# Performance work log

Hardware: AMD Instinct MI355X
Metric: run time of the kernel (lower is better)

The kernel has to match this reference:

```python
import jax, jax.numpy as jnp
import numpy as np

B, D = 90000, 100
E_GNN, E_MLP = 4, 4
E = E_GNN + E_MLP + 1  # 9
K = 2
NOISE_EPS = 0.01
LOSS_COEF = 0.4
GATE_MEAN, GATE_STD = 0.1, 1.0  # registered buffers in the torch module


def setup_inputs() -> dict:
    key = jax.random.key(0)
    ks = jax.random.split(key, 16)
    f = jax.random.normal
    return {
        "memory_feats": f(ks[0], (B, D), jnp.float32),
        "recent_raw": f(ks[1], (B, E_MLP, D), jnp.float32),
        "spatial_raw": f(ks[2], (B, E_GNN, D), jnp.float32),
        "node_feats_src": f(ks[3], (B, D), jnp.float32),
        "noise": f(ks[4], (B, E), jnp.float32),
        "deg_coef": f(ks[5], (1, D, 2), jnp.float32),
        "w_gate": f(ks[6], (6 * D, E), jnp.float32) * 0.05,
        "w_noise": f(ks[7], (6 * D, E), jnp.float32) * 0.05,
        "src_w": f(ks[8], (D, D), jnp.float32) * 0.1,
        "src_b": f(ks[9], (D,), jnp.float32) * 0.1,
        "dst_w": f(ks[10], (D, D), jnp.float32) * 0.1,
        "dst_b": f(ks[11], (D,), jnp.float32) * 0.1,
        "out_w": f(ks[12], (D, 1), jnp.float32) * 0.1,
        "out_b": f(ks[13], (1,), jnp.float32) * 0.1,
        "degree": jax.random.randint(ks[14], (B,), 0, 64, jnp.int32),
        "neg_samples": 1,
    }


def _cv_squared(x):
    # torch .var() is unbiased (ddof=1)
    return jnp.var(x, ddof=1) / (jnp.mean(x) ** 2 + 1e-10)


def _norm_cdf(v):
    return jax.scipy.stats.norm.cdf(v, loc=GATE_MEAN, scale=GATE_STD)


def reference(memory_feats, recent_raw, spatial_raw, node_feats_src, noise,
              deg_coef, w_gate, w_noise, src_w, src_b, dst_w, dst_b,
              out_w, out_b, degree, neg_samples):
    # memory expert output (dropout is identity in eval; relu applied)
    mem = jax.nn.relu(memory_feats)                        # [B, D]
    rec = jax.nn.relu(recent_raw)                          # [B, Em, D]
    log_deg = jnp.log(degree.astype(mem.dtype) + 1.0)      # [B]
    # degree-conditioned reweighting: stack([r, r*log_deg],-1) * deg_coef, sum(-1)
    c0, c1 = deg_coef[0, :, 0], deg_coef[0, :, 1]          # [D]
    spa = spatial_raw * (c0 + log_deg[:, None, None] * c1)  # [B, Eg, D]

    combine = jnp.concatenate([mem[:, None, :], spa, rec], axis=1)  # [B, E, D]
    result_spa = spa.mean(axis=1)
    result_rec = rec.mean(axis=1)
    x1 = mem + result_spa + result_rec
    x2 = mem * result_spa * result_rec
    cat = jnp.concatenate([mem, result_spa, result_rec, x1, x2, node_feats_src], axis=1)  # [B, 6D]

    # noisy top-k gating (train=True)
    clean = cat @ w_gate                                   # [B, E]
    std = jax.nn.softplus(cat @ w_noise) + NOISE_EPS
    noisy = clean + noise * std
    top_vals, top_idx = jax.lax.top_k(noisy, K + 1)        # [B, K+1]
    topk_gates = jax.nn.softmax(top_vals[:, :K], axis=1)
    b_idx = jnp.arange(noisy.shape[0])[:, None]
    gates = jnp.zeros_like(noisy).at[b_idx, top_idx[:, :K]].set(topk_gates)

    # prob of being in top-k for load-balance loss
    thr_in = top_vals[:, K][:, None]
    thr_out = top_vals[:, K - 1][:, None]
    is_in = noisy > thr_in
    prob = jnp.where(is_in,
                     _norm_cdf((clean - thr_in) / std),
                     _norm_cdf((clean - thr_out) / std))
    load = prob.sum(axis=0)
    importance = gates.sum(axis=0)
    loss = LOSS_COEF * (_cv_squared(importance) + _cv_squared(load))

    out = jnp.einsum('bed,be->bd', combine, gates)         # [B, D]

    # edge predictor
    num_edge = out.shape[0] // (neg_samples + 2)
    h_src = out[:num_edge] @ src_w + src_b
    h_pos = out[num_edge:2 * num_edge] @ dst_w + dst_b
    h_neg = out[2 * num_edge:] @ dst_w + dst_b
    pos = jax.nn.relu(h_src + h_pos) @ out_w + out_b       # [num_edge, 1]
    neg = jax.nn.relu(jnp.tile(h_src, (neg_samples, 1)) + h_neg) @ out_w + out_b
    return pos, neg, loss
```

## Files before the change

### kernel.cpp

```cpp
#include <hip/hip_runtime.h>
#include <math.h>

#define DD 100
#define GGATE 1024

#define DPP_ADD(v, ctrl) ((v) + __int_as_float(__builtin_amdgcn_update_dpp( \
    0, __float_as_int(v), (ctrl), 0xf, 0xf, true)))

__device__ __forceinline__ float blo(unsigned u){
  union { unsigned i; float f; } c; c.i = u << 16; return c.f;
}
__device__ __forceinline__ float bhi(unsigned u){
  union { unsigned i; float f; } c; c.i = u & 0xFFFF0000u; return c.f;
}
__device__ __forceinline__ unsigned short f2bf(float f){
  unsigned u = __float_as_uint(f);
  unsigned r = (u + 0x7FFFu + ((u >> 16) & 1u)) >> 16;
  return (unsigned short)r;
}
__device__ __forceinline__ float phi_fast(float z){
  float x  = z * 0.70710678118654752440f;
  float ax = fabsf(x);
  float t  = __builtin_amdgcn_rcpf(1.0f + 0.3275911f*ax);
  float p  = t*(0.254829592f + t*(-0.284496736f + t*(1.421413741f
           + t*(-1.453152027f + t*1.061405429f))));
  float e  = __expf(-ax*ax);
  float erfv = copysignf(1.0f - p*e, x);
  return 0.5f*(1.0f + erfv);
}
__device__ __forceinline__ float4 relu4(float4 v){
  return make_float4(fmaxf(v.x,0.f), fmaxf(v.y,0.f), fmaxf(v.z,0.f), fmaxf(v.w,0.f));
}

__global__ void k_fold(const float* __restrict__ wg, const float* __restrict__ wn,
                       float* __restrict__ wfold)
{
  int idx = blockIdx.x*256 + threadIdx.x;
  if (idx >= 9000) return;
  int dim = idx/90, r = idx%90, s = r/18, e = r%18;
  const float* W = (e < 9) ? wg : wn;
  int ee = (e < 9) ? e : e-9;
  int rowA = (s==0) ? dim : (s==1) ? 100+dim : (s==2) ? 200+dim
           : (s==3) ? 400+dim : 500+dim;
  float v = W[rowA*9 + ee] + ((s < 3) ? W[(300+dim)*9 + ee] : 0.f);
  wfold[idx] = v;
}

__global__ __launch_bounds__(256) void k_gate(
    const float* __restrict__ memf, const float* __restrict__ recr,
    const float* __restrict__ spar, const float* __restrict__ nsrc,
    const float* __restrict__ noise, const float* __restrict__ degc,
    const float* __restrict__ wfold, const int* __restrict__ degree,
    float4* __restrict__ gateinfo, float* __restrict__ partials, int B)
{
  __shared__ __align__(16) float sWF[100*92];
  __shared__ __align__(16) float sC0[DD], sC1[DD];
  __shared__ float sPart[4][18];

  for (int i = threadIdx.x; i < 9000; i += 256){
    int d = i/90, r = i%90;
    int slot = (d>>2) + 25*(d&3);
    sWF[slot*92 + r] = wfold[i];
  }
  for (int i = threadIdx.x; i < DD; i += 256){ sC0[i]=degc[2*i]; sC1[i]=degc[2*i+1]; }
  __syncthreads();

  const int wave = threadIdx.x >> 6, lane = threadIdx.x & 63;
  const int fq = lane & 3, rl = lane >> 2;
  const float4* sC04 = (const float4*)sC0;
  const float4* sC14 = (const float4*)sC1;

  float ldA[9], imA[9];
  #pragma unroll
  for (int e = 0; e < 9; e++){ ldA[e]=0.f; imA[e]=0.f; }

  const int ntile = (B + 63) / 64;
  for (int t = blockIdx.x; t < ntile; t += GGATE){
    const int row = t*64 + wave*16 + rl;
    const bool valid = row < B;
    const int rc = valid ? row : B-1;
    const float* pm = memf + (size_t)rc*DD;
    const float* ps = spar + (size_t)rc*4*DD;
    const float* pr = recr + (size_t)rc*4*DD;
    const float* pn = nsrc + (size_t)rc*DD;
    float ldg = __logf((float)degree[rc] + 1.0f);

    float cg[9], cn[9];
    #pragma unroll
    for (int e = 0; e < 9; e++){ cg[e]=0.f; cn[e]=0.f; }

    for (int k = 0; k < 7; k++){
      int c = fq + 4*k;
      float fz = (c < 25) ? 1.f : 0.f;
      int ce = (c < 25) ? c : 0;
      float4 me = *(const float4*)(pm + 4*ce);
      float4 s0 = *(const float4*)(ps + 0*DD + 4*ce);
      float4 s1 = *(const float4*)(ps + 1*DD + 4*ce);
      float4 s2 = *(const float4*)(ps + 2*DD + 4*ce);
      float4 s3 = *(const float4*)(ps + 3*DD + 4*ce);
      float4 r0 = *(const float4*)(pr + 0*DD + 4*ce);
      float4 r1 = *(const float4*)(pr + 1*DD + 4*ce);
      float4 r2 = *(const float4*)(pr + 2*DD + 4*ce);
      float4 r3 = *(const float4*)(pr + 3*DD + 4*ce);
      float4 nv = *(const float4*)(pn + 4*ce);
      float4 c04 = sC04[ce], c14 = sC14[ce];

      float4 m4 = relu4(me);
      float4 sc = make_float4(c04.x + ldg*c14.x, c04.y + ldg*c14.y,
                              c04.z + ldg*c14.z, c04.w + ldg*c14.w);
      float4 rs4 = make_float4((s0.x+s1.x+s2.x+s3.x)*0.25f*sc.x,
                               (s0.y+s1.y+s2.y+s3.y)*0.25f*sc.y,
                               (s0.z+s1.z+s2.z+s3.z)*0.25f*sc.z,
                               (s0.w+s1.w+s2.w+s3.w)*0.25f*sc.w);
      float4 a0 = relu4(r0), a1 = relu4(r1), a2 = relu4(r2), a3 = relu4(r3);
      float4 rr4 = make_float4((a0.x+a1.x+a2.x+a3.x)*0.25f,
                               (a0.y+a1.y+a2.y+a3.y)*0.25f,
                               (a0.z+a1.z+a2.z+a3.z)*0.25f,
                               (a0.w+a1.w+a2.w+a3.w)*0.25f);
      m4.x*=fz; m4.y*=fz; m4.z*=fz; m4.w*=fz;
      rs4.x*=fz; rs4.y*=fz; rs4.z*=fz; rs4.w*=fz;
      rr4.x*=fz; rr4.y*=fz; rr4.z*=fz; rr4.w*=fz;
      float4 ns4 = make_float4(nv.x*fz, nv.y*fz, nv.z*fz, nv.w*fz);
      float4 x24 = make_float4(m4.x*rs4.x*rr4.x, m4.y*rs4.y*rr4.y,
                               m4.z*rs4.z*rr4.z, m4.w*rs4.w*rr4.w);

      #pragma unroll
      for (int j = 0; j < 4; j++){
        const float der0 = (j==0)?m4.x :(j==1)?m4.y :(j==2)?m4.z :m4.w;
        const float der1 = (j==0)?rs4.x:(j==1)?rs4.y:(j==2)?rs4.z:rs4.w;
        const float der2 = (j==0)?rr4.x:(j==1)?rr4.y:(j==2)?rr4.z:rr4.w;
        const float der3 = (j==0)?x24.x:(j==1)?x24.y:(j==2)?x24.z:x24.w;
        const float der4 = (j==0)?ns4.x:(j==1)?ns4.y:(j==2)?ns4.z:ns4.w;
        const float4* wpj = (const float4*)(sWF + (ce + 25*j)*92);
        #pragma unroll
        for (int tq = 0; tq < 23; tq++){
          float4 w = wpj[tq];
          #pragma unroll
          for (int u = 0; u < 4; u++){
            const int ww = 4*tq + u;
            if (ww < 90){
              const int seg = ww/18, e = ww%18;
              float wv = (u==0)?w.x:(u==1)?w.y:(u==2)?w.z:w.w;
              float dv = (seg==0)?der0:(seg==1)?der1:(seg==2)?der2:(seg==3)?der3:der4;
              if (e < 9) cg[e] += dv*wv; else cn[e-9] += dv*wv;
            }
          }
        }
      }
    }

    #pragma unroll
    for (int e = 0; e < 9; e++){
      cg[e] = DPP_ADD(cg[e], 0xB1); cg[e] = DPP_ADD(cg[e], 0x4E);
      cn[e] = DPP_ADD(cn[e], 0xB1); cn[e] = DPP_ADD(cn[e], 0x4E);
    }

    float sd[9], rsd[9], nz[9];
    #pragma unroll
    for (int e = 0; e < 9; e++){
      float x = cn[e];
      float spl = fmaxf(x, 0.f) + __logf(1.0f + __expf(-fabsf(x)));
      sd[e]  = spl + 0.01f;
      rsd[e] = __builtin_amdgcn_rcpf(sd[e]);
      nz[e]  = cg[e] + noise[(size_t)rc*9 + e] * sd[e];
    }
    float v1 = -3.402823e38f, v2 = v1, v3 = v1; int i1 = -1, i2 = -1;
    #pragma unroll
    for (int e = 0; e < 9; e++){
      float v = nz[e];
      if (v > v1){ v3=v2; v2=v1; i2=i1; v1=v; i1=e; }
      else if (v > v2){ v3=v2; v2=v; i2=e; }
      else if (v > v3){ v3=v; }
    }
    float tt = __expf(v2 - v1);
    float g1 = __builtin_amdgcn_rcpf(1.0f + tt);
    float g2 = tt*g1;
    if (valid){
      #pragma unroll
      for (int e = 0; e < 9; e++){
        float thr = (nz[e] > v3) ? v3 : v2;
        float z = (cg[e] - thr)*rsd[e] - 0.1f;
        ldA[e] += phi_fast(z);
        imA[e] += (e==i1) ? g1 : ((e==i2) ? g2 : 0.f);
      }
      if (fq == 0)
        gateinfo[row] = make_float4(g1, g2, __int_as_float(i1), __int_as_float(i2));
    }
  }

  #pragma unroll
  for (int e = 0; e < 9; e++){
    #pragma unroll
    for (int off = 4; off < 64; off <<= 1){
      ldA[e] += __shfl_xor(ldA[e], off, 64);
      imA[e] += __shfl_xor(imA[e], off, 64);
    }
  }
  if (lane == 0){
    #pragma unroll
    for (int e = 0; e < 9; e++){ sPart[wave][e] = imA[e]; sPart[wave][9+e] = ldA[e]; }
  }
  __syncthreads();
  if (threadIdx.x < 18){
    float s = sPart[0][threadIdx.x] + sPart[1][threadIdx.x]
            + sPart[2][threadIdx.x] + sPart[3][threadIdx.x];
    partials[blockIdx.x*18 + threadIdx.x] = s;
  }
}

__global__ __launch_bounds__(256) void k_mix(
    const float* __restrict__ memf, const float* __restrict__ recr,
    const float* __restrict__ spar, const float* __restrict__ degc,
    const int* __restrict__ degree, const float4* __restrict__ gateinfo,
    float* __restrict__ outm, int B)
{
  const int total = B*25;
  for (int idx = blockIdx.x*256 + threadIdx.x; idx < total; idx += gridDim.x*256){
    int row = idx / 25, q = idx - row*25;
    float4 gi = gateinfo[row];
    float gv[2] = {gi.x, gi.y};
    int   ei[2] = {__float_as_int(gi.z), __float_as_int(gi.w)};
    float4 acc = make_float4(0.f,0.f,0.f,0.f);
    #pragma unroll
    for (int s = 0; s < 2; s++){
      int e = ei[s]; float g = gv[s];
      float4 v;
      if (e == 0){
        v = relu4(*(const float4*)(memf + (size_t)row*DD + 4*q));
      } else if (e < 5){
        float ldg = __logf((float)degree[row] + 1.0f);
        float4 ca = *(const float4*)(degc + 8*q);
        float4 cb = *(const float4*)(degc + 8*q + 4);
        float4 sv = *(const float4*)(spar + ((size_t)row*4 + (e-1))*DD + 4*q);
        v = make_float4(sv.x*(ca.x + ldg*ca.y), sv.y*(ca.z + ldg*ca.w),
                        sv.z*(cb.x + ldg*cb.y), sv.w*(cb.z + ldg*cb.w));
      } else {
        v = relu4(*(const float4*)(recr + ((size_t)row*4 + (e-5))*DD + 4*q));
      }
      acc.x += g*v.x; acc.y += g*v.y; acc.z += g*v.z; acc.w += g*v.w;
    }
    ((float4*)outm)[(size_t)row*25 + q] = acc;
  }
}

__global__ __launch_bounds__(1024) void k_loss(const float* __restrict__ partials,
                                               int nblk, float* __restrict__ dloss)
{
  __shared__ float sS[18][57];
  int t = threadIdx.x;
  if (t < 1008){
    int k = t % 18, c = t / 18;
    float s = 0.f;
    for (int b = c; b < nblk; b += 56) s += partials[b*18 + k];
    sS[k][c] = s;
  }
  __syncthreads();
  if (t < 18){
    float tot = 0.f;
    #pragma unroll
    for (int c = 0; c < 56; c++) tot += sS[t][c];
    sS[t][56] = tot;
  }
  __syncthreads();
  if (t == 0){
    float mi = 0.f, ml = 0.f;
    #pragma unroll
    for (int e = 0; e < 9; e++){ mi += sS[e][56]; ml += sS[9+e][56]; }
    mi *= (1.f/9.f); ml *= (1.f/9.f);
    float vi = 0.f, vl = 0.f;
    #pragma unroll
    for (int e = 0; e < 9; e++){
      float a = sS[e][56]   - mi; vi += a*a;
      float b = sS[9+e][56] - ml; vl += b*b;
    }
    vi *= (1.f/8.f); vl *= (1.f/8.f);
    *dloss = 0.4f * (vi/(mi*mi + 1e-10f) + vl/(ml*ml + 1e-10f));
  }
}

__global__ __launch_bounds__(512) void k_edge(
    const float* __restrict__ om,
    const float* __restrict__ sw, const float* __restrict__ sb,
    const float* __restrict__ dw, const float* __restrict__ db,
    const float* __restrict__ ow, const float* __restrict__ ob,
    float* __restrict__ dout, int NE)
{
  __shared__ __align__(4) unsigned short sSW[DD*102];
  __shared__ __align__(4) unsigned short sDW[DD*102];
  __shared__ float sSB[DD], sDB[DD], sOW[DD];

  for (int i = threadIdx.x; i < DD*DD; i += 512){
    int k = i / DD, d = i % DD;
    sSW[d*102 + k] = f2bf(sw[i]);
    sDW[d*102 + k] = f2bf(dw[i]);
  }
  for (int i = threadIdx.x; i < DD; i += 512){ sSB[i]=sb[i]; sDB[i]=db[i]; sOW[i]=ow[i]; }
  __syncthreads();

  const int wave = threadIdx.x >> 6, lane = threadIdx.x & 63;
  const int grp = blockIdx.x*8 + wave;
  const int e0 = grp*4;
  if (e0 >= NE) return;
  const int e0u = __builtin_amdgcn_readfirstlane(e0);
  const float* oS = om + (size_t)e0u*DD;
  const float* oP = om + ((size_t)(NE  + e0u))*DD;
  const float* oN = om + ((size_t)(2*NE + e0u))*DD;
  const int d0 = lane, d1 = lane + 64;
  const bool h1 = (d1 < DD);
  const int dc1 = h1 ? d1 : 0;

  float aS[4][2], aP[4][2], aN[4][2];
  #pragma unroll
  for (int r = 0; r < 4; r++){
    aS[r][0]=0.f; aS[r][1]=0.f; aP[r][0]=0.f; aP[r][1]=0.f; aN[r][0]=0.f; aN[r][1]=0.f;
  }

  for (int k = 0; k < DD; k += 4){
    unsigned uA = *(const unsigned*)&sSW[d0 *102 + k];
    unsigned uB = *(const unsigned*)&sSW[d0 *102 + k + 2];
    unsigned uC = *(const unsigned*)&sSW[dc1*102 + k];
    unsigned uD = *(const unsigned*)&sSW[dc1*102 + k + 2];
    unsigned uE = *(const unsigned*)&sDW[d0 *102 + k];
    unsigned uF = *(const unsigned*)&sDW[d0 *102 + k + 2];
    unsigned uG = *(const unsigned*)&sDW[dc1*102 + k];
    unsigned uH = *(const unsigned*)&sDW[dc1*102 + k + 2];
    float wS00=blo(uA), wS01=bhi(uA), wS02=blo(uB), wS03=bhi(uB);
    float wS10=blo(uC), wS11=bhi(uC), wS12=blo(uD), wS13=bhi(uD);
    float wD00=blo(uE), wD01=bhi(uE), wD02=blo(uF), wD03=bhi(uF);
    float wD10=blo(uG), wD11=bhi(uG), wD12=blo(uH), wD13=bhi(uH);
    #pragma unroll
    for (int r = 0; r < 4; r++){
      float4 ov = *(const float4*)(oS + r*DD + k);
      float4 pv = *(const float4*)(oP + r*DD + k);
      float4 nv = *(const float4*)(oN + r*DD + k);
      aS[r][0] += ov.x*wS00 + ov.y*wS01 + ov.z*wS02 + ov.w*wS03;
      aS[r][1] += ov.x*wS10 + ov.y*wS11 + ov.z*wS12 + ov.w*wS13;
      aP[r][0] += pv.x*wD00 + pv.y*wD01 + pv.z*wD02 + pv.w*wD03;
      aP[r][1] += pv.x*wD10 + pv.y*wD11 + pv.z*wD12 + pv.w*wD13;
      aN[r][0] += nv.x*wD00 + nv.y*wD01 + nv.z*wD02 + nv.w*wD03;
      aN[r][1] += nv.x*wD10 + nv.y*wD11 + nv.z*wD12 + nv.w*wD13;
    }
  }

  float owa = sOW[d0], owb = sOW[dc1];
  float sba = sSB[d0], sbb = sSB[dc1];
  float dba = sDB[d0], dbb = sDB[dc1];
  float ob0 = ob[0];
  #pragma unroll
  for (int r = 0; r < 4; r++){
    float hs0 = aS[r][0] + sba, hp0 = aP[r][0] + dba, hn0 = aN[r][0] + dba;
    float tp = fmaxf(hs0 + hp0, 0.f)*owa;
    float tn = fmaxf(hs0 + hn0, 0.f)*owa;
    if (h1){
      float hs1 = aS[r][1] + sbb, hp1 = aP[r][1] + dbb, hn1 = aN[r][1] + dbb;
      tp += fmaxf(hs1 + hp1, 0.f)*owb;
      tn += fmaxf(hs1 + hn1, 0.f)*owb;
    }
    #pragma unroll
    for (int off = 32; off > 0; off >>= 1){
      tp += __shfl_xor(tp, off, 64);
      tn += __shfl_xor(tn, off, 64);
    }
    if (lane == 0){
      dout[e0 + r]      = tp + ob0;
      dout[NE + e0 + r] = tn + ob0;
    }
  }
}

extern "C" void kernel_launch(void* const* d_in, const int* in_sizes, int n_in,
                              void* d_out, int out_size, void* d_ws, size_t ws_size,
                              hipStream_t stream)
{
  (void)n_in; (void)out_size; (void)ws_size;
  const float* memf  = (const float*)d_in[0];
  const float* recr  = (const float*)d_in[1];
  const float* spar  = (const float*)d_in[2];
  const float* nsrc  = (const float*)d_in[3];
  const float* noise = (const float*)d_in[4];
  const float* degc  = (const float*)d_in[5];
  const float* wg    = (const float*)d_in[6];
  const float* wn    = (const float*)d_in[7];
  const float* sw    = (const float*)d_in[8];
  const float* sb    = (const float*)d_in[9];
  const float* dw    = (const float*)d_in[10];
  const float* db    = (const float*)d_in[11];
  const float* ow    = (const float*)d_in[12];
  const float* ob    = (const float*)d_in[13];
  const int*   deg   = (const int*)d_in[14];

  const int B  = in_sizes[0] / DD;
  const int NE = B / 3;

  float4* gateinfo = (float4*)d_ws;
  float*  outm     = (float*)(gateinfo + B);
  float*  partials = outm + (size_t)B*DD;
  float*  wfold    = partials + (size_t)GGATE*18;
  float*  dout     = (float*)d_out;

  k_fold<<<dim3(36), dim3(256), 0, stream>>>(wg, wn, wfold);
  k_gate<<<dim3(GGATE), dim3(256), 0, stream>>>(memf, recr, spar, nsrc, noise,
                                                degc, wfold, deg, gateinfo,
                                                partials, B);
  k_mix<<<dim3(2048), dim3(256), 0, stream>>>(memf, recr, spar, degc, deg,
                                              gateinfo, outm, B);
  k_loss<<<dim3(1), dim3(1024), 0, stream>>>(partials, GGATE, dout + 2*NE);
  const int blocks2 = (NE/4 + 7) / 8;
  k_edge<<<dim3(blocks2), dim3(512), 0, stream>>>(outm, sw, sb, dw, db, ow, ob, dout, NE);
}
```

Measured before the change: 257.1 us.

## Fuse expert mixing into gating kernel and software-prefetch next input chunk

Removes the separate k_mix kernel and the gateinfo buffer. Each row's gated mixture is now computed inside k_gate right after top-k selection, while the row's data is likely still in cache. The 7-step feature loop also double-buffers its global loads, issuing the next chunk's ten float4 loads before the FMA-heavy inner work, with the loop kept rolled. This saves one launch and a global round trip of the inputs, at the cost of more register pressure in k_gate and mixing stores done by only some lanes.

```diff
diff --git a/kernel.cpp b/kernel.cpp
--- a/kernel.cpp
+++ b/kernel.cpp
@@ -46,12 +46,24 @@
   wfold[idx] = v;
 }
 
+#define LOADL(CE) \
+  Lme = *(const float4*)(pm + 4*(CE)); \
+  Ls0 = *(const float4*)(ps + 0*DD + 4*(CE)); \
+  Ls1 = *(const float4*)(ps + 1*DD + 4*(CE)); \
+  Ls2 = *(const float4*)(ps + 2*DD + 4*(CE)); \
+  Ls3 = *(const float4*)(ps + 3*DD + 4*(CE)); \
+  Lr0 = *(const float4*)(pr + 0*DD + 4*(CE)); \
+  Lr1 = *(const float4*)(pr + 1*DD + 4*(CE)); \
+  Lr2 = *(const float4*)(pr + 2*DD + 4*(CE)); \
+  Lr3 = *(const float4*)(pr + 3*DD + 4*(CE)); \
+  Lnv = *(const float4*)(pn + 4*(CE));
+
 __global__ __launch_bounds__(256) void k_gate(
     const float* __restrict__ memf, const float* __restrict__ recr,
     const float* __restrict__ spar, const float* __restrict__ nsrc,
     const float* __restrict__ noise, const float* __restrict__ degc,
     const float* __restrict__ wfold, const int* __restrict__ degree,
-    float4* __restrict__ gateinfo, float* __restrict__ partials, int B)
+    float* __restrict__ outm, float* __restrict__ partials, int B)
 {
   __shared__ __align__(16) float sWF[100*92];
   __shared__ __align__(16) float sC0[DD], sC1[DD];
@@ -89,30 +101,24 @@
     #pragma unroll
     for (int e = 0; e < 9; e++){ cg[e]=0.f; cn[e]=0.f; }
 
+    float4 Lme, Ls0, Ls1, Ls2, Ls3, Lr0, Lr1, Lr2, Lr3, Lnv;
+    LOADL(fq)
+
+    #pragma unroll 1
     for (int k = 0; k < 7; k++){
-      int c = fq + 4*k;
-      float fz = (c < 25) ? 1.f : 0.f;
-      int ce = (c < 25) ? c : 0;
-      float4 me = *(const float4*)(pm + 4*ce);
-      float4 s0 = *(const float4*)(ps + 0*DD + 4*ce);
-      float4 s1 = *(const float4*)(ps + 1*DD + 4*ce);
-      float4 s2 = *(const float4*)(ps + 2*DD + 4*ce);
-      float4 s3 = *(const float4*)(ps + 3*DD + 4*ce);
-      float4 r0 = *(const float4*)(pr + 0*DD + 4*ce);
-      float4 r1 = *(const float4*)(pr + 1*DD + 4*ce);
-      float4 r2 = *(const float4*)(pr + 2*DD + 4*ce);
-      float4 r3 = *(const float4*)(pr + 3*DD + 4*ce);
-      float4 nv = *(const float4*)(pn + 4*ce);
+      const int c = fq + 4*k;
+      const float fz = (c < 25) ? 1.f : 0.f;
+      const int ce = (c < 25) ? c : 0;
+
       float4 c04 = sC04[ce], c14 = sC14[ce];
-
-      float4 m4 = relu4(me);
+      float4 m4 = relu4(Lme);
       float4 sc = make_float4(c04.x + ldg*c14.x, c04.y + ldg*c14.y,
                               c04.z + ldg*c14.z, c04.w + ldg*c14.w);
-      float4 rs4 = make_float4((s0.x+s1.x+s2.x+s3.x)*0.25f*sc.x,
-                               (s0.y+s1.y+s2.y+s3.y)*0.25f*sc.y,
-                               (s0.z+s1.z+s2.z+s3.z)*0.25f*sc.z,
-                               (s0.w+s1.w+s2.w+s3.w)*0.25f*sc.w);
-      float4 a0 = relu4(r0), a1 = relu4(r1), a2 = relu4(r2), a3 = relu4(r3);
+      float4 rs4 = make_float4((Ls0.x+Ls1.x+Ls2.x+Ls3.x)*0.25f*sc.x,
+                               (Ls0.y+Ls1.y+Ls2.y+Ls3.y)*0.25f*sc.y,
+                               (Ls0.z+Ls1.z+Ls2.z+Ls3.z)*0.25f*sc.z,
+                               (Ls0.w+Ls1.w+Ls2.w+Ls3.w)*0.25f*sc.w);
+      float4 a0 = relu4(Lr0), a1 = relu4(Lr1), a2 = relu4(Lr2), a3 = relu4(Lr3);
       float4 rr4 = make_float4((a0.x+a1.x+a2.x+a3.x)*0.25f,
                                (a0.y+a1.y+a2.y+a3.y)*0.25f,
                                (a0.z+a1.z+a2.z+a3.z)*0.25f,
@@ -120,9 +126,14 @@
       m4.x*=fz; m4.y*=fz; m4.z*=fz; m4.w*=fz;
       rs4.x*=fz; rs4.y*=fz; rs4.z*=fz; rs4.w*=fz;
       rr4.x*=fz; rr4.y*=fz; rr4.z*=fz; rr4.w*=fz;
-      float4 ns4 = make_float4(nv.x*fz, nv.y*fz, nv.z*fz, nv.w*fz);
+      float4 ns4 = make_float4(Lnv.x*fz, Lnv.y*fz, Lnv.z*fz, Lnv.w*fz);
       float4 x24 = make_float4(m4.x*rs4.x*rr4.x, m4.y*rs4.y*rr4.y,
                                m4.z*rs4.z*rr4.z, m4.w*rs4.w*rr4.w);
+
+      const int kn  = (k < 6) ? k+1 : 6;
+      const int cn2 = fq + 4*kn;
+      const int cen = (cn2 < 25) ? cn2 : 0;
+      LOADL(cen)
 
       #pragma unroll
       for (int j = 0; j < 4; j++){
@@ -183,8 +194,33 @@
         ldA[e] += phi_fast(z);
         imA[e] += (e==i1) ? g1 : ((e==i2) ? g2 : 0.f);
       }
-      if (fq == 0)
-        gateinfo[row] = make_float4(g1, g2, __int_as_float(i1), __int_as_float(i2));
+
+      float* po = outm + (size_t)rc*DD;
+      #pragma unroll
+      for (int k2 = 0; k2 < 7; k2++){
+        const int c2 = fq + 4*k2;
+        if (c2 < 25){
+          float4 acc = make_float4(0.f,0.f,0.f,0.f);
+          #pragma unroll
+          for (int s2 = 0; s2 < 2; s2++){
+            const int ei = s2 ? i2 : i1;
+            const float g = s2 ? g2 : g1;
+            float4 v;
+            if (ei == 0){
+              v = relu4(*(const float4*)(pm + 4*c2));
+            } else if (ei < 5){
+              float4 sv = *(const float4*)(ps + (ei-1)*DD + 4*c2);
+              float4 c04 = sC04[c2], c14 = sC14[c2];
+              v = make_float4(sv.x*(c04.x + ldg*c14.x), sv.y*(c04.y + ldg*c14.y),
+                              sv.z*(c04.z + ldg*c14.z), sv.w*(c04.w + ldg*c14.w));
+            } else {
+              v = relu4(*(const float4*)(pr + (ei-5)*DD + 4*c2));
+            }
+            acc.x += g*v.x; acc.y += g*v.y; acc.z += g*v.z; acc.w += g*v.w;
+          }
+          *(float4*)(po + 4*c2) = acc;
+        }
+      }
     }
   }
 
@@ -205,41 +241,6 @@
     float s = sPart[0][threadIdx.x] + sPart[1][threadIdx.x]
             + sPart[2][threadIdx.x] + sPart[3][threadIdx.x];
     partials[blockIdx.x*18 + threadIdx.x] = s;
-  }
-}
-
-__global__ __launch_bounds__(256) void k_mix(
-    const float* __restrict__ memf, const float* __restrict__ recr,
-    const float* __restrict__ spar, const float* __restrict__ degc,
-    const int* __restrict__ degree, const float4* __restrict__ gateinfo,
-    float* __restrict__ outm, int B)
-{
-  const int total = B*25;
-  for (int idx = blockIdx.x*256 + threadIdx.x; idx < total; idx += gridDim.x*256){
-    int row = idx / 25, q = idx - row*25;
-    float4 gi = gateinfo[row];
-    float gv[2] = {gi.x, gi.y};
-    int   ei[2] = {__float_as_int(gi.z), __float_as_int(gi.w)};
-    float4 acc = make_float4(0.f,0.f,0.f,0.f);
-    #pragma unroll
-    for (int s = 0; s < 2; s++){
-      int e = ei[s]; float g = gv[s];
-      float4 v;
-      if (e == 0){
-        v = relu4(*(const float4*)(memf + (size_t)row*DD + 4*q));
-      } else if (e < 5){
-        float ldg = __logf((float)degree[row] + 1.0f);
-        float4 ca = *(const float4*)(degc + 8*q);
-        float4 cb = *(const float4*)(degc + 8*q + 4);
-        float4 sv = *(const float4*)(spar + ((size_t)row*4 + (e-1))*DD + 4*q);
-        v = make_float4(sv.x*(ca.x + ldg*ca.y), sv.y*(ca.z + ldg*ca.w),
-                        sv.z*(cb.x + ldg*cb.y), sv.w*(cb.z + ldg*cb.w));
-      } else {
-        v = relu4(*(const float4*)(recr + ((size_t)row*4 + (e-5))*DD + 4*q));
-      }
-      acc.x += g*v.x; acc.y += g*v.y; acc.z += g*v.z; acc.w += g*v.w;
-    }
-    ((float4*)outm)[(size_t)row*25 + q] = acc;
   }
 }
 
@@ -392,18 +393,15 @@
   const int B  = in_sizes[0] / DD;
   const int NE = B / 3;
 
-  float4* gateinfo = (float4*)d_ws;
-  float*  outm     = (float*)(gateinfo + B);
+  float*  outm     = (float*)d_ws;
   float*  partials = outm + (size_t)B*DD;
   float*  wfold    = partials + (size_t)GGATE*18;
   float*  dout     = (float*)d_out;
 
   k_fold<<<dim3(36), dim3(256), 0, stream>>>(wg, wn, wfold);
   k_gate<<<dim3(GGATE), dim3(256), 0, stream>>>(memf, recr, spar, nsrc, noise,
-                                                degc, wfold, deg, gateinfo,
+                                                degc, wfold, deg, outm,
                                                 partials, B);
-  k_mix<<<dim3(2048), dim3(256), 0, stream>>>(memf, recr, spar, degc, deg,
-                                              gateinfo, outm, B);
   k_loss<<<dim3(1), dim3(1024), 0, stream>>>(partials, GGATE, dout + 2*NE);
   const int blocks2 = (NE/4 + 7) / 8;
   k_edge<<<dim3(blocks2), dim3(512), 0, stream>>>(outm, sw, sb, dw, db, ow, ob, dout, NE);
```

Result: slower. 297.0 us (+15.5%).
